# Performance work log

Measured on AMD Instinct MI355X. Metric: run time of the kernel, lower is better.

Reference implementation:

```python
import jax, jax.numpy as jnp
import numpy as np

B, T, A, F_IN = 32, 128, 22, 32
H1, C1 = 4, 128  # heads, gnn_hidden_dim
NEG_SLOPE = 0.2  # GATConv default leaky_relu slope


def setup_inputs() -> dict:
    key = jax.random.key(0)
    ks = jax.random.split(key, 12)
    g = lambda k, shape: jax.random.normal(k, shape, dtype=jnp.float32) * 0.05
    d1 = H1 * C1  # 512, concat output dim of multi-head layers
    return {
        "features": jax.random.normal(ks[0], (B, T, A, F_IN), dtype=jnp.float32),
        "W1": g(ks[1], (F_IN, H1, C1)), "as1": g(ks[2], (H1, C1)), "ad1": g(ks[3], (H1, C1)), "b1": jnp.zeros((d1,), jnp.float32),
        "W2": g(ks[4], (d1, H1, C1)), "as2": g(ks[5], (H1, C1)), "ad2": g(ks[6], (H1, C1)), "b2": jnp.zeros((d1,), jnp.float32),
        "W3": g(ks[7], (d1, 1, C1)), "as3": g(ks[8], (1, C1)), "ad3": g(ks[9], (1, C1)), "b3": jnp.zeros((C1,), jnp.float32),
        "Wc": g(ks[10], (C1, 1)), "bc": jnp.zeros((1,), jnp.float32),
    }


def _gat(x, W, a_src, a_dst, b, concat):
    # x: [G, A, F]; complete graph + self loops == dense attention over all A nodes.
    h = jnp.einsum('gaf,fhc->gahc', x, W)           # [G, A, H, C]
    s = jnp.einsum('gahc,hc->gha', h, a_src)        # att_src . h_j
    d = jnp.einsum('gahc,hc->gha', h, a_dst)        # att_dst . h_i
    logits = d[:, :, :, None] + s[:, :, None, :]    # [G, H, i, j] edge j->i
    logits = jnp.where(logits >= 0, logits, NEG_SLOPE * logits)
    alpha = jax.nn.softmax(logits, axis=-1)         # softmax over source nodes j
    out = jnp.einsum('ghij,gjhc->gihc', alpha, h)   # [G, A, H, C]
    G_, A_, H_, C_ = out.shape
    out = out.reshape(G_, A_, H_ * C_) if concat else out.mean(axis=2)
    return out + b


def reference(features, W1, as1, ad1, b1, W2, as2, ad2, b2, W3, as3, ad3, b3, Wc, bc):
    Bb, Tt, Aa, Ff = features.shape
    x = features.reshape(Bb * Tt, Aa, Ff)           # [G, A, F], G = B*T frame-graphs
    x = jax.nn.relu(_gat(x, W1, as1, ad1, b1, True))
    x = jax.nn.relu(_gat(x, W2, as2, ad2, b2, True))
    x = jax.nn.relu(_gat(x, W3, as3, ad3, b3, False))
    pooled = x.mean(axis=1)                         # global_mean_pool over 22 agents
    return (pooled @ Wc + bc)[:, 0]                 # [G] logits
```

## Files before the change

kernel.cpp:

```cpp
#include <hip/hip_runtime.h>

typedef unsigned short u16;
typedef unsigned int   u32;
typedef unsigned long long u64;
typedef short bf16x8 __attribute__((ext_vector_type(8)));
typedef float f32x4  __attribute__((ext_vector_type(4)));
typedef u32   u32x4  __attribute__((ext_vector_type(4)));

#define NA 22
#define FIN 32
#define XS_STR 520
#define AL_STR 24

#define W1_OFF 0
#define W2_OFF 16384
#define W3_OFF 278528
#define E1_OFF 344064
#define E2_OFF 344576
#define E3_OFF 352768
#define WS_TOTAL 360960

__device__ float b2f(u16 u) {
    return __uint_as_float(((unsigned int)u) << 16);
}

__device__ u16 f2b(float f) {
    unsigned int x = __float_as_uint(f);
    x = (x + 0x7fffu + ((x >> 16) & 1u)) >> 16;
    return (u16)x;
}

__device__ __forceinline__ u32 cvtpk(float lo, float hi) {
    u32 r;
    asm("v_cvt_pk_bf16_f32 %0, %1, %2" : "=v"(r) : "v"(lo), "v"(hi));
    return r;
}

__global__ void swizzle_kernel(const float* W1, const float* W2, const float* W3, u16* ws)
{
    int t = blockIdx.x * 256 + threadIdx.x;
    const float* W; int NT, nshift, base, loc;
    if (t < W2_OFF)      { W = W1; NT = 32; nshift = 9; base = W1_OFF; loc = t; }
    else if (t < W3_OFF) { W = W2; NT = 32; nshift = 9; base = W2_OFF; loc = t - W2_OFF; }
    else if (t < E1_OFF) { W = W3; NT = 8;  nshift = 7; base = W3_OFF; loc = t - W3_OFF; }
    else { return; }
    int k = loc >> nshift;
    int n = loc & ((1 << nshift) - 1);
    u16 v = f2b(W[loc]);
    int kt = k >> 5, quad = (k & 31) >> 3, j = k & 7;
    int nt = n >> 4, lm = n & 15;
    int lane = (quad << 4) | lm;
    ws[base + (((kt * NT + nt) << 9) | (lane << 3) | j)] = v;
}

__global__ void wav_kernel(const float* W1, const float* as1, const float* ad1,
                           const float* W2, const float* as2, const float* ad2,
                           const float* W3, const float* as3, const float* ad3,
                           u16* ws)
{
    int t = blockIdx.x * 256 + threadIdx.x;
    const float* W; const float* asp; const float* adp;
    int H, N, base, loc;
    if (t < 512)        { W = W1; asp = as1; adp = ad1; H = 4; N = 512; base = E1_OFF; loc = t; }
    else if (t < 8704)  { W = W2; asp = as2; adp = ad2; H = 4; N = 512; base = E2_OFF; loc = t - 512; }
    else if (t < 16896) { W = W3; asp = as3; adp = ad3; H = 1; N = 128; base = E3_OFF; loc = t - 8704; }
    else { return; }
    int kt = loc >> 9, r = loc & 511;
    int lane = r >> 3, j = r & 7;
    int quad = lane >> 4, lm = lane & 15;
    u16 outv = 0;
    if (lm < 2 * H) {
        int h = (H == 4) ? (lm & 3) : 0;
        int which = (H == 4) ? (lm >> 2) : lm;
        const float* av = which ? adp : asp;
        int k = kt * 32 + quad * 8 + j;
        float s = 0.f;
        for (int c = 0; c < 128; ++c) { s += W[k * N + h * 128 + c] * av[h * 128 + c]; }
        outv = f2b(s);
    }
    ws[base + (kt << 9) + (lane << 3) + j] = outv;
}


template<int KT, int NT, int NTW, int H>
__device__ __forceinline__ void gat_layer(
    const u16* Wsw, const u16* Wext, const float* bias,
    u16* xs, float* svw, u16* al)
{
    int tid  = threadIdx.x;
    int wave = tid >> 6, lane = tid & 63;
    int quad = lane >> 4, lm = lane & 15;
    int r1 = 16 + lm; if (r1 >= NA) { r1 = lm; }

    f32x4 acc0[NTW], acc1[NTW], accE0, accE1;

    {
        const u16* a0base = xs + lm * XS_STR + quad * 8;
        const u16* a1base = xs + r1 * XS_STR + quad * 8;
        const u16* wbase  = Wsw + ((wave * NTW) << 9) + (lane << 3);
        const u16* ebase  = Wext + (lane << 3);

        f32x4 z4 = {0.f, 0.f, 0.f, 0.f};
        #pragma unroll
        for (int n = 0; n < NTW; ++n) { acc0[n] = z4; acc1[n] = z4; }
        accE0 = z4; accE1 = z4;

        bf16x8 bbuf[2][NTW], ebuf[2], ab0[2], ab1[2];
        #pragma unroll
        for (int n = 0; n < NTW; ++n) { bbuf[0][n] = *(const bf16x8*)(wbase + (n << 9)); }
        ebuf[0] = *(const bf16x8*)(ebase);
        ab0[0] = *(const bf16x8*)(a0base);
        ab1[0] = *(const bf16x8*)(a1base);

        #pragma unroll
        for (int kt = 0; kt < KT; ++kt) {
            const int cur = kt & 1;
            const int nxt = cur ^ 1;
            if (kt + 1 < KT) {
                const u16* wn = wbase + (((kt + 1) * NT) << 9);
                #pragma unroll
                for (int n = 0; n < NTW; ++n) { bbuf[nxt][n] = *(const bf16x8*)(wn + (n << 9)); }
                ebuf[nxt] = *(const bf16x8*)(ebase + ((kt + 1) << 9));
                ab0[nxt] = *(const bf16x8*)(a0base + (kt + 1) * 32);
                ab1[nxt] = *(const bf16x8*)(a1base + (kt + 1) * 32);
            }
            #pragma unroll
            for (int n = 0; n < NTW; ++n) {
                acc0[n] = __builtin_amdgcn_mfma_f32_16x16x32_bf16(ab0[cur], bbuf[cur][n], acc0[n], 0, 0, 0);
                acc1[n] = __builtin_amdgcn_mfma_f32_16x16x32_bf16(ab1[cur], bbuf[cur][n], acc1[n], 0, 0, 0);
            }
            accE0 = __builtin_amdgcn_mfma_f32_16x16x32_bf16(ab0[cur], ebuf[cur], accE0, 0, 0, 0);
            accE1 = __builtin_amdgcn_mfma_f32_16x16x32_bf16(ab1[cur], ebuf[cur], accE1, 0, 0, 0);
        }
    }

    int head = (H == 4) ? (wave >> 1) : 0;
    float* sw = svw + wave * 48;
    if (lm == head) {
        #pragma unroll
        for (int r = 0; r < 4; ++r) {
            sw[quad * 4 + r] = accE0[r];
            int row1 = 16 + quad * 4 + r;
            if (row1 < NA) { sw[row1] = accE1[r]; }
        }
    }
    if (lm == head + H) {
        #pragma unroll
        for (int r = 0; r < 4; ++r) {
            sw[24 + quad * 4 + r] = accE0[r];
            int row1 = 16 + quad * 4 + r;
            if (row1 < NA) { sw[24 + row1] = accE1[r]; }
        }
    }

    bf16x8 bfrag[NTW];
    {
        int s0 = (((quad & 1) << 5) | lm) << 2;
        int s2 = s0 + 64;
        bool hi = (quad >= 2);
        #pragma unroll
        for (int n = 0; n < NTW; ++n) {
            u32 P0a = cvtpk(acc0[n][0], acc0[n][1]);
            u32 P1a = cvtpk(acc0[n][2], acc0[n][3]);
            u32 P0b = cvtpk(acc1[n][0], acc1[n][1]);
            u32 P1b = cvtpk(acc1[n][2], acc1[n][3]);
            u32 w0a = (u32)__builtin_amdgcn_ds_bpermute(s0, (int)P0a);
            u32 w0b = (u32)__builtin_amdgcn_ds_bpermute(s0, (int)P0b);
            u32 w1a = (u32)__builtin_amdgcn_ds_bpermute(s0, (int)P1a);
            u32 w1b = (u32)__builtin_amdgcn_ds_bpermute(s0, (int)P1b);
            u32 w2a = (u32)__builtin_amdgcn_ds_bpermute(s2, (int)P0a);
            u32 w2b = (u32)__builtin_amdgcn_ds_bpermute(s2, (int)P0b);
            u32 w3a = (u32)__builtin_amdgcn_ds_bpermute(s2, (int)P1a);
            union { u32 w[4]; bf16x8 v; } bu;
            bu.w[0] = hi ? w0b : w0a;
            bu.w[1] = hi ? w1b : w1a;
            bu.w[2] = hi ? w2b : w2a;
            bu.w[3] = hi ? 0u  : w3a;
            bfrag[n] = bu.v;
        }
    }

    if (lane < NA) {
        float di = sw[24 + lane];
        float lg[NA];
        float mx = -1.0e30f, ss = 0.0f;
        #pragma unroll
        for (int j = 0; j < NA; ++j) {
            float l = di + sw[j];
            l = fmaxf(l, 0.2f * l);
            lg[j] = l;
            mx = fmaxf(mx, l);
        }
        #pragma unroll
        for (int j = 0; j < NA; ++j) {
            float e = __expf(lg[j] - mx);
            lg[j] = e;
            ss += e;
        }
        float inv = 1.0f / ss;
        u32 pk[12];
        #pragma unroll
        for (int j2 = 0; j2 < 11; ++j2) {
            pk[j2] = cvtpk(lg[2 * j2] * inv, lg[2 * j2 + 1] * inv);
        }
        pk[11] = 0;
        u32* arow = (u32*)(al + (wave * NA + lane) * AL_STR);
        u32x4 q0 = {pk[0], pk[1], pk[2],  pk[3]};
        u32x4 q1 = {pk[4], pk[5], pk[6],  pk[7]};
        u32x4 q2 = {pk[8], pk[9], pk[10], pk[11]};
        *(u32x4*)(arow)     = q0;
        *(u32x4*)(arow + 4) = q1;
        *(u32x4*)(arow + 8) = q2;
    }

    const u16* albase = al + wave * NA * AL_STR;
    bf16x8 zb = {0, 0, 0, 0, 0, 0, 0, 0};
    bf16x8 pa0 = (quad < 3) ? *(const bf16x8*)(albase + lm * AL_STR + quad * 8) : zb;
    bf16x8 pa1 = (quad < 3) ? *(const bf16x8*)(albase + r1 * AL_STR + quad * 8) : zb;

    f32x4 agg0[NTW], agg1[NTW];
    f32x4 z4 = {0.f, 0.f, 0.f, 0.f};
    float bv[NTW];
    #pragma unroll
    for (int n = 0; n < NTW; ++n) {
        int col = (wave * NTW + n) * 16 + lm;
        bv[n] = bias[col];
        agg0[n] = __builtin_amdgcn_mfma_f32_16x16x32_bf16(pa0, bfrag[n], z4, 0, 0, 0);
        agg1[n] = __builtin_amdgcn_mfma_f32_16x16x32_bf16(pa1, bfrag[n], z4, 0, 0, 0);
    }

    __syncthreads();

    #pragma unroll
    for (int n = 0; n < NTW; ++n) {
        int col = (wave * NTW + n) * 16 + lm;
        u16* cbase = xs + col;
        float v0 = fmaxf(agg0[n][0] + bv[n], 0.0f);
        float v1 = fmaxf(agg0[n][1] + bv[n], 0.0f);
        float v2 = fmaxf(agg0[n][2] + bv[n], 0.0f);
        float v3 = fmaxf(agg0[n][3] + bv[n], 0.0f);
        u32 wa0 = cvtpk(v0, v1), wa1 = cvtpk(v2, v3);
        int r0 = quad * 4;
        cbase[(r0 + 0) * XS_STR] = (u16)wa0;
        cbase[(r0 + 1) * XS_STR] = (u16)(wa0 >> 16);
        cbase[(r0 + 2) * XS_STR] = (u16)wa1;
        cbase[(r0 + 3) * XS_STR] = (u16)(wa1 >> 16);
        if (quad < 2) {
            float u0 = fmaxf(agg1[n][0] + bv[n], 0.0f);
            float u1 = fmaxf(agg1[n][1] + bv[n], 0.0f);
            u32 wb0 = cvtpk(u0, u1);
            int r16 = 16 + quad * 4;
            cbase[(r16 + 0) * XS_STR] = (u16)wb0;
            cbase[(r16 + 1) * XS_STR] = (u16)(wb0 >> 16);
            if (quad == 0) {
                float u2 = fmaxf(agg1[n][2] + bv[n], 0.0f);
                float u3 = fmaxf(agg1[n][3] + bv[n], 0.0f);
                u32 wb1 = cvtpk(u2, u3);
                cbase[18 * XS_STR] = (u16)wb1;
                cbase[19 * XS_STR] = (u16)(wb1 >> 16);
            }
        }
    }
    __syncthreads();
}

template<int KT, int NT>
__device__ __forceinline__ void gat_final(
    const u16* Wsw, const u16* Wext, const float* bias,
    const u16* xs, float* svw, u16* al,
    const float* Wc, const float* bc, float* partial, float* out, int g)
{
    int tid  = threadIdx.x;
    int wave = tid >> 6, lane = tid & 63;
    int quad = lane >> 4, lm = lane & 15;
    int r1 = 16 + lm; if (r1 >= NA) { r1 = lm; }

    f32x4 acc0, acc1, accE0, accE1;

    {
        const u16* a0base = xs + lm * XS_STR + quad * 8;
        const u16* a1base = xs + r1 * XS_STR + quad * 8;
        const u16* wbase  = Wsw + (wave << 9) + (lane << 3);
        const u16* ebase  = Wext + (lane << 3);

        f32x4 z4 = {0.f, 0.f, 0.f, 0.f};
        acc0 = z4; acc1 = z4; accE0 = z4; accE1 = z4;

        bf16x8 bbuf[2], ebuf[2], ab0[2], ab1[2];
        bbuf[0] = *(const bf16x8*)(wbase);
        ebuf[0] = *(const bf16x8*)(ebase);
        ab0[0] = *(const bf16x8*)(a0base);
        ab1[0] = *(const bf16x8*)(a1base);

        #pragma unroll
        for (int kt = 0; kt < KT; ++kt) {
            const int cur = kt & 1;
            const int nxt = cur ^ 1;
            if (kt + 1 < KT) {
                bbuf[nxt] = *(const bf16x8*)(wbase + (((kt + 1) * NT) << 9));
                ebuf[nxt] = *(const bf16x8*)(ebase + ((kt + 1) << 9));
                ab0[nxt] = *(const bf16x8*)(a0base + (kt + 1) * 32);
                ab1[nxt] = *(const bf16x8*)(a1base + (kt + 1) * 32);
            }
            acc0  = __builtin_amdgcn_mfma_f32_16x16x32_bf16(ab0[cur], bbuf[cur], acc0, 0, 0, 0);
            acc1  = __builtin_amdgcn_mfma_f32_16x16x32_bf16(ab1[cur], bbuf[cur], acc1, 0, 0, 0);
            accE0 = __builtin_amdgcn_mfma_f32_16x16x32_bf16(ab0[cur], ebuf[cur], accE0, 0, 0, 0);
            accE1 = __builtin_amdgcn_mfma_f32_16x16x32_bf16(ab1[cur], ebuf[cur], accE1, 0, 0, 0);
        }
    }

    float* sw = svw + wave * 48;
    if (lm == 0) {
        #pragma unroll
        for (int r = 0; r < 4; ++r) {
            sw[quad * 4 + r] = accE0[r];
            int row1 = 16 + quad * 4 + r;
            if (row1 < NA) { sw[row1] = accE1[r]; }
        }
    }
    if (lm == 1) {
        #pragma unroll
        for (int r = 0; r < 4; ++r) {
            sw[24 + quad * 4 + r] = accE0[r];
            int row1 = 16 + quad * 4 + r;
            if (row1 < NA) { sw[24 + row1] = accE1[r]; }
        }
    }

    bf16x8 bfrag;
    {
        int s0 = (((quad & 1) << 5) | lm) << 2;
        int s2 = s0 + 64;
        bool hi = (quad >= 2);
        u32 P0a = cvtpk(acc0[0], acc0[1]);
        u32 P1a = cvtpk(acc0[2], acc0[3]);
        u32 P0b = cvtpk(acc1[0], acc1[1]);
        u32 P1b = cvtpk(acc1[2], acc1[3]);
        u32 w0a = (u32)__builtin_amdgcn_ds_bpermute(s0, (int)P0a);
        u32 w0b = (u32)__builtin_amdgcn_ds_bpermute(s0, (int)P0b);
        u32 w1a = (u32)__builtin_amdgcn_ds_bpermute(s0, (int)P1a);
        u32 w1b = (u32)__builtin_amdgcn_ds_bpermute(s0, (int)P1b);
        u32 w2a = (u32)__builtin_amdgcn_ds_bpermute(s2, (int)P0a);
        u32 w2b = (u32)__builtin_amdgcn_ds_bpermute(s2, (int)P0b);
        u32 w3a = (u32)__builtin_amdgcn_ds_bpermute(s2, (int)P1a);
        union { u32 w[4]; bf16x8 v; } bu;
        bu.w[0] = hi ? w0b : w0a;
        bu.w[1] = hi ? w1b : w1a;
        bu.w[2] = hi ? w2b : w2a;
        bu.w[3] = hi ? 0u  : w3a;
        bfrag = bu.v;
    }

    if (lane < NA) {
        float di = sw[24 + lane];
        float lg[NA];
        float mx = -1.0e30f, ss = 0.0f;
        #pragma unroll
        for (int j = 0; j < NA; ++j) {
            float l = di + sw[j];
            l = fmaxf(l, 0.2f * l);
            lg[j] = l;
            mx = fmaxf(mx, l);
        }
        #pragma unroll
        for (int j = 0; j < NA; ++j) {
            float e = __expf(lg[j] - mx);
            lg[j] = e;
            ss += e;
        }
        float inv = 1.0f / ss;
        u32 pk[12];
        #pragma unroll
        for (int j2 = 0; j2 < 11; ++j2) {
            pk[j2] = cvtpk(lg[2 * j2] * inv, lg[2 * j2 + 1] * inv);
        }
        pk[11] = 0;
        u32* arow = (u32*)(al + (wave * NA + lane) * AL_STR);
        u32x4 q0 = {pk[0], pk[1], pk[2],  pk[3]};
        u32x4 q1 = {pk[4], pk[5], pk[6],  pk[7]};
        u32x4 q2 = {pk[8], pk[9], pk[10], pk[11]};
        *(u32x4*)(arow)     = q0;
        *(u32x4*)(arow + 4) = q1;
        *(u32x4*)(arow + 8) = q2;
    }

    const u16* albase = al + wave * NA * AL_STR;
    bf16x8 zb = {0, 0, 0, 0, 0, 0, 0, 0};
    bf16x8 pa0 = (quad < 3) ? *(const bf16x8*)(albase + lm * AL_STR + quad * 8) : zb;
    bf16x8 pa1 = (quad < 3) ? *(const bf16x8*)(albase + r1 * AL_STR + quad * 8) : zb;

    f32x4 z4 = {0.f, 0.f, 0.f, 0.f};
    f32x4 agg0 = __builtin_amdgcn_mfma_f32_16x16x32_bf16(pa0, bfrag, z4, 0, 0, 0);
    f32x4 agg1 = __builtin_amdgcn_mfma_f32_16x16x32_bf16(pa1, bfrag, z4, 0, 0, 0);

    int col = wave * 16 + lm;
    float bvv = bias[col];
    float cs = 0.0f;
    #pragma unroll
    for (int r = 0; r < 4; ++r) { cs += fmaxf(agg0[r] + bvv, 0.0f); }
    #pragma unroll
    for (int r = 0; r < 4; ++r) {
        int row1 = 16 + quad * 4 + r;
        if (row1 < NA) { cs += fmaxf(agg1[r] + bvv, 0.0f); }
    }
    cs += __shfl_xor(cs, 16);
    cs += __shfl_xor(cs, 32);
    float part = (cs / 22.0f) * Wc[col];
    part += __shfl_xor(part, 1);
    part += __shfl_xor(part, 2);
    part += __shfl_xor(part, 4);
    part += __shfl_xor(part, 8);
    if (lane == 0) { partial[wave] = part; }
    __syncthreads();
    if (tid == 0) {
        float t = 0.0f;
        #pragma unroll
        for (int w = 0; w < 8; ++w) { t += partial[w]; }
        out[g] = t + bc[0];
    }
}

__global__ void __launch_bounds__(512, 3)
pressgnn_kernel(const float* feats, const u16* ws,
                const float* b1, const float* b2, const float* b3,
                const float* Wc, const float* bc,
                float* out)
{
    __shared__ __align__(16) u16 xs[NA * XS_STR];
    __shared__ __align__(16) u16 al[8 * NA * AL_STR];
    __shared__ __align__(16) float svw[8 * 48];
    __shared__ float partial[8];

    int g = blockIdx.x;
    int tid = threadIdx.x;

    for (int i = tid; i < NA * FIN; i += 512) {
        int row = i >> 5;
        int col = i & 31;
        xs[row * XS_STR + col] = f2b(feats[g * NA * FIN + i]);
    }
    __syncthreads();

    gat_layer<1,  32, 4, 4>(ws + W1_OFF, ws + E1_OFF, b1, xs, svw, al);
    gat_layer<16, 32, 4, 4>(ws + W2_OFF, ws + E2_OFF, b2, xs, svw, al);
    gat_final<16, 8>(ws + W3_OFF, ws + E3_OFF, b3, xs, svw, al,
                     Wc, bc, partial, out, g);
}

extern "C" void kernel_launch(void* const* d_in, const int* in_sizes, int n_in,
                              void* d_out, int out_size, void* d_ws, size_t ws_size,
                              hipStream_t stream) {
    const float* feats = (const float*)d_in[0];
    const float* W1  = (const float*)d_in[1];
    const float* as1 = (const float*)d_in[2];
    const float* ad1 = (const float*)d_in[3];
    const float* b1  = (const float*)d_in[4];
    const float* W2  = (const float*)d_in[5];
    const float* as2 = (const float*)d_in[6];
    const float* ad2 = (const float*)d_in[7];
    const float* b2  = (const float*)d_in[8];
    const float* W3  = (const float*)d_in[9];
    const float* as3 = (const float*)d_in[10];
    const float* ad3 = (const float*)d_in[11];
    const float* b3  = (const float*)d_in[12];
    const float* Wc  = (const float*)d_in[13];
    const float* bc  = (const float*)d_in[14];
    float* out = (float*)d_out;
    u16* ws = (u16*)d_ws;

    swizzle_kernel<<<dim3(1344), dim3(256), 0, stream>>>(W1, W2, W3, ws);
    wav_kernel<<<dim3(66), dim3(256), 0, stream>>>(W1, as1, ad1, W2, as2, ad2,
                                                   W3, as3, ad3, ws);

    pressgnn_kernel<<<dim3(out_size), dim3(512), 0, stream>>>(
        feats, ws, b1, b2, b3, Wc, bc, out);
}
```

Before: 254.1 us.

## Process two frame-graphs per 1024-thread block to reuse weight fragments

The main kernel now handles two graphs per block with 16 waves. Each weight B-fragment loaded from global memory feeds MFMAs for both graphs, which halves weight traffic per graph. Attention logit MFMAs and softmax run only on lead waves, and the attention matrices are shared across waves through LDS behind an extra barrier. The wav precompute kernel is also rewritten to use wave-parallel dot products with shuffle reductions instead of serial 128-length loops per thread. The cost is a larger block, a bigger LDS footprint and more synchronisation, which may reduce occupancy.

```diff
diff --git a/kernel.cpp b/kernel.cpp
--- a/kernel.cpp
+++ b/kernel.cpp
@@ -10,6 +10,7 @@
 #define NA 22
 #define FIN 32
 #define XS_STR 520
+#define XS_G (NA * XS_STR)
 #define AL_STR 24
 
 #define W1_OFF 0
@@ -19,10 +20,6 @@
 #define E2_OFF 344576
 #define E3_OFF 352768
 #define WS_TOTAL 360960
-
-__device__ float b2f(u16 u) {
-    return __uint_as_float(((unsigned int)u) << 16);
-}
 
 __device__ u16 f2b(float f) {
     unsigned int x = __float_as_uint(f);
@@ -58,32 +55,115 @@
                            const float* W3, const float* as3, const float* ad3,
                            u16* ws)
 {
-    int t = blockIdx.x * 256 + threadIdx.x;
-    const float* W; const float* asp; const float* adp;
-    int H, N, base, loc;
-    if (t < 512)        { W = W1; asp = as1; adp = ad1; H = 4; N = 512; base = E1_OFF; loc = t; }
-    else if (t < 8704)  { W = W2; asp = as2; adp = ad2; H = 4; N = 512; base = E2_OFF; loc = t - 512; }
-    else if (t < 16896) { W = W3; asp = as3; adp = ad3; H = 1; N = 128; base = E3_OFF; loc = t - 8704; }
-    else { return; }
-    int kt = loc >> 9, r = loc & 511;
-    int lane = r >> 3, j = r & 7;
-    int quad = lane >> 4, lm = lane & 15;
-    u16 outv = 0;
-    if (lm < 2 * H) {
-        int h = (H == 4) ? (lm & 3) : 0;
-        int which = (H == 4) ? (lm >> 2) : lm;
-        const float* av = which ? adp : asp;
-        int k = kt * 32 + quad * 8 + j;
-        float s = 0.f;
-        for (int c = 0; c < 128; ++c) { s += W[k * N + h * 128 + c] * av[h * 128 + c]; }
-        outv = f2b(s);
-    }
-    ws[base + (kt << 9) + (lane << 3) + j] = outv;
-}
-
-
-template<int KT, int NT, int NTW, int H>
-__device__ __forceinline__ void gat_layer(
+    int wid = blockIdx.x * 4 + (threadIdx.x >> 6);
+    int lane = threadIdx.x & 63;
+    int grp = lane >> 4, c4 = lane & 15;
+
+    if (wid < 544) {
+        const float* W; const float* asp; const float* adp; int k, base;
+        if (wid < 32) { W = W1; asp = as1; adp = ad1; k = wid;      base = E1_OFF; }
+        else          { W = W2; asp = as2; adp = ad2; k = wid - 32; base = E2_OFF; }
+        int h = grp;
+        const float4* wp = (const float4*)(W + k * 512 + lane * 8);
+        float4 wa = wp[0], wb = wp[1];
+        const float4* sp = (const float4*)(asp + h * 128 + c4 * 8);
+        const float4* dp = (const float4*)(adp + h * 128 + c4 * 8);
+        float4 sa = sp[0], sb = sp[1];
+        float4 da = dp[0], db = dp[1];
+        float ps = wa.x*sa.x + wa.y*sa.y + wa.z*sa.z + wa.w*sa.w
+                 + wb.x*sb.x + wb.y*sb.y + wb.z*sb.z + wb.w*sb.w;
+        float pd = wa.x*da.x + wa.y*da.y + wa.z*da.z + wa.w*da.w
+                 + wb.x*db.x + wb.y*db.y + wb.z*db.z + wb.w*db.w;
+        #pragma unroll
+        for (int off = 1; off <= 8; off <<= 1) {
+            ps += __shfl_xor(ps, off);
+            pd += __shfl_xor(pd, off);
+        }
+        int kt = k >> 5, quad = (k & 31) >> 3, j = k & 7;
+        if (c4 < 4) {
+            int col = c4 * 4 + h;
+            float v = (c4 == 0) ? ps : (c4 == 1) ? pd : 0.0f;
+            ws[base + (kt << 9) + (((quad << 4) | col) << 3) + j] = f2b(v);
+        }
+    } else if (wid < 672) {
+        int k = (wid - 544) * 4 + grp;
+        const float4* wp = (const float4*)(W3 + k * 128 + c4 * 8);
+        float4 wa = wp[0], wb = wp[1];
+        const float4* sp = (const float4*)(as3 + c4 * 8);
+        const float4* dp = (const float4*)(ad3 + c4 * 8);
+        float4 sa = sp[0], sb = sp[1];
+        float4 da = dp[0], db = dp[1];
+        float ps = wa.x*sa.x + wa.y*sa.y + wa.z*sa.z + wa.w*sa.w
+                 + wb.x*sb.x + wb.y*sb.y + wb.z*sb.z + wb.w*sb.w;
+        float pd = wa.x*da.x + wa.y*da.y + wa.z*da.z + wa.w*da.w
+                 + wb.x*db.x + wb.y*db.y + wb.z*db.z + wb.w*db.w;
+        #pragma unroll
+        for (int off = 1; off <= 8; off <<= 1) {
+            ps += __shfl_xor(ps, off);
+            pd += __shfl_xor(pd, off);
+        }
+        int kt = k >> 5, quad = (k & 31) >> 3, j = k & 7;
+        float v = (c4 == 0) ? ps : (c4 == 1) ? pd : 0.0f;
+        ws[E3_OFF + (kt << 9) + (((quad << 4) | c4) << 3) + j] = f2b(v);
+    }
+}
+
+__device__ __forceinline__ bf16x8 xpose(f32x4 a0, f32x4 a1, int s0, int s2, bool hi)
+{
+    u32 P0a = cvtpk(a0[0], a0[1]);
+    u32 P1a = cvtpk(a0[2], a0[3]);
+    u32 P0b = cvtpk(a1[0], a1[1]);
+    u32 P1b = cvtpk(a1[2], a1[3]);
+    u32 w0a = (u32)__builtin_amdgcn_ds_bpermute(s0, (int)P0a);
+    u32 w0b = (u32)__builtin_amdgcn_ds_bpermute(s0, (int)P0b);
+    u32 w1a = (u32)__builtin_amdgcn_ds_bpermute(s0, (int)P1a);
+    u32 w1b = (u32)__builtin_amdgcn_ds_bpermute(s0, (int)P1b);
+    u32 w2a = (u32)__builtin_amdgcn_ds_bpermute(s2, (int)P0a);
+    u32 w2b = (u32)__builtin_amdgcn_ds_bpermute(s2, (int)P0b);
+    u32 w3a = (u32)__builtin_amdgcn_ds_bpermute(s2, (int)P1a);
+    union { u32 w[4]; bf16x8 v; } bu;
+    bu.w[0] = hi ? w0b : w0a;
+    bu.w[1] = hi ? w1b : w1a;
+    bu.w[2] = hi ? w2b : w2a;
+    bu.w[3] = hi ? 0u  : w3a;
+    return bu.v;
+}
+
+__device__ __forceinline__ void softmax_al(const float* sw, u16* al_slot, int lane)
+{
+    if (lane < NA) {
+        float di = sw[24 + lane];
+        float lg[NA];
+        float mx = -1.0e30f, ss = 0.0f;
+        #pragma unroll
+        for (int j = 0; j < NA; ++j) {
+            float l = di + sw[j];
+            l = fmaxf(l, 0.2f * l);
+            lg[j] = l;
+            mx = fmaxf(mx, l);
+        }
+        #pragma unroll
+        for (int j = 0; j < NA; ++j) {
+            float e = __expf(lg[j] - mx);
+            lg[j] = e;
+            ss += e;
+        }
+        float inv = 1.0f / ss;
+        u32 pk[12];
+        #pragma unroll
+        for (int j2 = 0; j2 < 11; ++j2) {
+            pk[j2] = cvtpk(lg[2 * j2] * inv, lg[2 * j2 + 1] * inv);
+        }
+        pk[11] = 0;
+        u32* arow = (u32*)(al_slot + lane * AL_STR);
+        *(u32x4*)(arow)     = (u32x4){pk[0], pk[1], pk[2],  pk[3]};
+        *(u32x4*)(arow + 4) = (u32x4){pk[4], pk[5], pk[6],  pk[7]};
+        *(u32x4*)(arow + 8) = (u32x4){pk[8], pk[9], pk[10], pk[11]};
+    }
+}
+
+template<int KT, int NT>
+__device__ __forceinline__ void gat_layer2(
     const u16* Wsw, const u16* Wext, const float* bias,
     u16* xs, float* svw, u16* al)
 {
@@ -91,26 +171,33 @@
     int wave = tid >> 6, lane = tid & 63;
     int quad = lane >> 4, lm = lane & 15;
     int r1 = 16 + lm; if (r1 >= NA) { r1 = lm; }
-
-    f32x4 acc0[NTW], acc1[NTW], accE0, accE1;
+    bool lead = (wave < 8);
+    int gl = wave & 1, hl = wave >> 1;
+
+    f32x4 acc0[2][2], acc1[2][2], accE0, accE1;
 
     {
-        const u16* a0base = xs + lm * XS_STR + quad * 8;
-        const u16* a1base = xs + r1 * XS_STR + quad * 8;
-        const u16* wbase  = Wsw + ((wave * NTW) << 9) + (lane << 3);
-        const u16* ebase  = Wext + (lane << 3);
+        const u16* a00 = xs + lm * XS_STR + quad * 8;
+        const u16* a10 = xs + r1 * XS_STR + quad * 8;
+        const u16* wbase = Wsw + ((wave * 2) << 9) + (lane << 3);
+        const u16* ebase = Wext + (lane << 3);
 
         f32x4 z4 = {0.f, 0.f, 0.f, 0.f};
         #pragma unroll
-        for (int n = 0; n < NTW; ++n) { acc0[n] = z4; acc1[n] = z4; }
+        for (int g = 0; g < 2; ++g) {
+            acc0[g][0] = z4; acc0[g][1] = z4;
+            acc1[g][0] = z4; acc1[g][1] = z4;
+        }
         accE0 = z4; accE1 = z4;
 
-        bf16x8 bbuf[2][NTW], ebuf[2], ab0[2], ab1[2];
-        #pragma unroll
-        for (int n = 0; n < NTW; ++n) { bbuf[0][n] = *(const bf16x8*)(wbase + (n << 9)); }
-        ebuf[0] = *(const bf16x8*)(ebase);
-        ab0[0] = *(const bf16x8*)(a0base);
-        ab1[0] = *(const bf16x8*)(a1base);
+        bf16x8 bbuf[2][2], ebuf[2], ab0[2][2], ab1[2][2];
+        bbuf[0][0] = *(const bf16x8*)(wbase);
+        bbuf[0][1] = *(const bf16x8*)(wbase + 512);
+        if (lead) { ebuf[0] = *(const bf16x8*)(ebase); }
+        ab0[0][0] = *(const bf16x8*)(a00);
+        ab1[0][0] = *(const bf16x8*)(a10);
+        ab0[0][1] = *(const bf16x8*)(a00 + XS_G);
+        ab1[0][1] = *(const bf16x8*)(a10 + XS_G);
 
         #pragma unroll
         for (int kt = 0; kt < KT; ++kt) {
@@ -118,179 +205,142 @@
             const int nxt = cur ^ 1;
             if (kt + 1 < KT) {
                 const u16* wn = wbase + (((kt + 1) * NT) << 9);
+                bbuf[nxt][0] = *(const bf16x8*)(wn);
+                bbuf[nxt][1] = *(const bf16x8*)(wn + 512);
+                if (lead) { ebuf[nxt] = *(const bf16x8*)(ebase + ((kt + 1) << 9)); }
+                ab0[nxt][0] = *(const bf16x8*)(a00 + (kt + 1) * 32);
+                ab1[nxt][0] = *(const bf16x8*)(a10 + (kt + 1) * 32);
+                ab0[nxt][1] = *(const bf16x8*)(a00 + XS_G + (kt + 1) * 32);
+                ab1[nxt][1] = *(const bf16x8*)(a10 + XS_G + (kt + 1) * 32);
+            }
+            #pragma unroll
+            for (int g = 0; g < 2; ++g) {
                 #pragma unroll
-                for (int n = 0; n < NTW; ++n) { bbuf[nxt][n] = *(const bf16x8*)(wn + (n << 9)); }
-                ebuf[nxt] = *(const bf16x8*)(ebase + ((kt + 1) << 9));
-                ab0[nxt] = *(const bf16x8*)(a0base + (kt + 1) * 32);
-                ab1[nxt] = *(const bf16x8*)(a1base + (kt + 1) * 32);
-            }
+                for (int n = 0; n < 2; ++n) {
+                    acc0[g][n] = __builtin_amdgcn_mfma_f32_16x16x32_bf16(ab0[cur][g], bbuf[cur][n], acc0[g][n], 0, 0, 0);
+                    acc1[g][n] = __builtin_amdgcn_mfma_f32_16x16x32_bf16(ab1[cur][g], bbuf[cur][n], acc1[g][n], 0, 0, 0);
+                }
+            }
+            if (lead) {
+                bf16x8 ea0 = gl ? ab0[cur][1] : ab0[cur][0];
+                bf16x8 ea1 = gl ? ab1[cur][1] : ab1[cur][0];
+                accE0 = __builtin_amdgcn_mfma_f32_16x16x32_bf16(ea0, ebuf[cur], accE0, 0, 0, 0);
+                accE1 = __builtin_amdgcn_mfma_f32_16x16x32_bf16(ea1, ebuf[cur], accE1, 0, 0, 0);
+            }
+        }
+    }
+
+    if (lead) {
+        float* sw = svw + wave * 48;
+        if (lm == hl) {
             #pragma unroll
-            for (int n = 0; n < NTW; ++n) {
-                acc0[n] = __builtin_amdgcn_mfma_f32_16x16x32_bf16(ab0[cur], bbuf[cur][n], acc0[n], 0, 0, 0);
-                acc1[n] = __builtin_amdgcn_mfma_f32_16x16x32_bf16(ab1[cur], bbuf[cur][n], acc1[n], 0, 0, 0);
-            }
-            accE0 = __builtin_amdgcn_mfma_f32_16x16x32_bf16(ab0[cur], ebuf[cur], accE0, 0, 0, 0);
-            accE1 = __builtin_amdgcn_mfma_f32_16x16x32_bf16(ab1[cur], ebuf[cur], accE1, 0, 0, 0);
-        }
-    }
-
-    int head = (H == 4) ? (wave >> 1) : 0;
-    float* sw = svw + wave * 48;
-    if (lm == head) {
-        #pragma unroll
-        for (int r = 0; r < 4; ++r) {
-            sw[quad * 4 + r] = accE0[r];
-            int row1 = 16 + quad * 4 + r;
-            if (row1 < NA) { sw[row1] = accE1[r]; }
-        }
-    }
-    if (lm == head + H) {
-        #pragma unroll
-        for (int r = 0; r < 4; ++r) {
-            sw[24 + quad * 4 + r] = accE0[r];
-            int row1 = 16 + quad * 4 + r;
-            if (row1 < NA) { sw[24 + row1] = accE1[r]; }
-        }
-    }
-
-    bf16x8 bfrag[NTW];
+            for (int r = 0; r < 4; ++r) {
+                sw[quad * 4 + r] = accE0[r];
+                int row1 = 16 + quad * 4 + r;
+                if (row1 < NA) { sw[row1] = accE1[r]; }
+            }
+        }
+        if (lm == hl + 4) {
+            #pragma unroll
+            for (int r = 0; r < 4; ++r) {
+                sw[24 + quad * 4 + r] = accE0[r];
+                int row1 = 16 + quad * 4 + r;
+                if (row1 < NA) { sw[24 + row1] = accE1[r]; }
+            }
+        }
+        softmax_al(sw, al + (gl * 4 + hl) * NA * AL_STR, lane);
+    }
+
+    bf16x8 bfrag[2][2];
     {
         int s0 = (((quad & 1) << 5) | lm) << 2;
         int s2 = s0 + 64;
         bool hi = (quad >= 2);
         #pragma unroll
-        for (int n = 0; n < NTW; ++n) {
-            u32 P0a = cvtpk(acc0[n][0], acc0[n][1]);
-            u32 P1a = cvtpk(acc0[n][2], acc0[n][3]);
-            u32 P0b = cvtpk(acc1[n][0], acc1[n][1]);
-            u32 P1b = cvtpk(acc1[n][2], acc1[n][3]);
-            u32 w0a = (u32)__builtin_amdgcn_ds_bpermute(s0, (int)P0a);
-            u32 w0b = (u32)__builtin_amdgcn_ds_bpermute(s0, (int)P0b);
-            u32 w1a = (u32)__builtin_amdgcn_ds_bpermute(s0, (int)P1a);
-            u32 w1b = (u32)__builtin_amdgcn_ds_bpermute(s0, (int)P1b);
-            u32 w2a = (u32)__builtin_amdgcn_ds_bpermute(s2, (int)P0a);
-            u32 w2b = (u32)__builtin_amdgcn_ds_bpermute(s2, (int)P0b);
-            u32 w3a = (u32)__builtin_amdgcn_ds_bpermute(s2, (int)P1a);
-            union { u32 w[4]; bf16x8 v; } bu;
-            bu.w[0] = hi ? w0b : w0a;
-            bu.w[1] = hi ? w1b : w1a;
-            bu.w[2] = hi ? w2b : w2a;
-            bu.w[3] = hi ? 0u  : w3a;
-            bfrag[n] = bu.v;
-        }
-    }
-
-    if (lane < NA) {
-        float di = sw[24 + lane];
-        float lg[NA];
-        float mx = -1.0e30f, ss = 0.0f;
-        #pragma unroll
-        for (int j = 0; j < NA; ++j) {
-            float l = di + sw[j];
-            l = fmaxf(l, 0.2f * l);
-            lg[j] = l;
-            mx = fmaxf(mx, l);
-        }
-        #pragma unroll
-        for (int j = 0; j < NA; ++j) {
-            float e = __expf(lg[j] - mx);
-            lg[j] = e;
-            ss += e;
-        }
-        float inv = 1.0f / ss;
-        u32 pk[12];
-        #pragma unroll
-        for (int j2 = 0; j2 < 11; ++j2) {
-            pk[j2] = cvtpk(lg[2 * j2] * inv, lg[2 * j2 + 1] * inv);
-        }
-        pk[11] = 0;
-        u32* arow = (u32*)(al + (wave * NA + lane) * AL_STR);
-        u32x4 q0 = {pk[0], pk[1], pk[2],  pk[3]};
-        u32x4 q1 = {pk[4], pk[5], pk[6],  pk[7]};
-        u32x4 q2 = {pk[8], pk[9], pk[10], pk[11]};
-        *(u32x4*)(arow)     = q0;
-        *(u32x4*)(arow + 4) = q1;
-        *(u32x4*)(arow + 8) = q2;
-    }
-
-    const u16* albase = al + wave * NA * AL_STR;
-    bf16x8 zb = {0, 0, 0, 0, 0, 0, 0, 0};
-    bf16x8 pa0 = (quad < 3) ? *(const bf16x8*)(albase + lm * AL_STR + quad * 8) : zb;
-    bf16x8 pa1 = (quad < 3) ? *(const bf16x8*)(albase + r1 * AL_STR + quad * 8) : zb;
-
-    f32x4 agg0[NTW], agg1[NTW];
-    f32x4 z4 = {0.f, 0.f, 0.f, 0.f};
-    float bv[NTW];
+        for (int g = 0; g < 2; ++g) {
+            bfrag[g][0] = xpose(acc0[g][0], acc1[g][0], s0, s2, hi);
+            bfrag[g][1] = xpose(acc0[g][1], acc1[g][1], s0, s2, hi);
+        }
+    }
+
+    __syncthreads();
+
+    int head = wave >> 2;
     #pragma unroll
-    for (int n = 0; n < NTW; ++n) {
-        int col = (wave * NTW + n) * 16 + lm;
-        bv[n] = bias[col];
-        agg0[n] = __builtin_amdgcn_mfma_f32_16x16x32_bf16(pa0, bfrag[n], z4, 0, 0, 0);
-        agg1[n] = __builtin_amdgcn_mfma_f32_16x16x32_bf16(pa1, bfrag[n], z4, 0, 0, 0);
-    }
-
+    for (int g = 0; g < 2; ++g) {
+        const u16* alb = al + (g * 4 + head) * NA * AL_STR;
+        bf16x8 zb = {0, 0, 0, 0, 0, 0, 0, 0};
+        bf16x8 pa0 = (quad < 3) ? *(const bf16x8*)(alb + lm * AL_STR + quad * 8) : zb;
+        bf16x8 pa1 = (quad < 3) ? *(const bf16x8*)(alb + r1 * AL_STR + quad * 8) : zb;
+        u16* xg = xs + g * XS_G;
+        #pragma unroll
+        for (int n = 0; n < 2; ++n) {
+            int col = (wave * 2 + n) * 16 + lm;
+            float bv = bias[col];
+            f32x4 z4 = {0.f, 0.f, 0.f, 0.f};
+            f32x4 agg0 = __builtin_amdgcn_mfma_f32_16x16x32_bf16(pa0, bfrag[g][n], z4, 0, 0, 0);
+            f32x4 agg1 = __builtin_amdgcn_mfma_f32_16x16x32_bf16(pa1, bfrag[g][n], z4, 0, 0, 0);
+            u16* cbase = xg + col;
+            float v0 = fmaxf(agg0[0] + bv, 0.0f);
+            float v1 = fmaxf(agg0[1] + bv, 0.0f);
+            float v2 = fmaxf(agg0[2] + bv, 0.0f);
+            float v3 = fmaxf(agg0[3] + bv, 0.0f);
+            u32 wa0 = cvtpk(v0, v1), wa1 = cvtpk(v2, v3);
+            int r0 = quad * 4;
+            cbase[(r0 + 0) * XS_STR] = (u16)wa0;
+            cbase[(r0 + 1) * XS_STR] = (u16)(wa0 >> 16);
+            cbase[(r0 + 2) * XS_STR] = (u16)wa1;
+            cbase[(r0 + 3) * XS_STR] = (u16)(wa1 >> 16);
+            if (quad < 2) {
+                float u0 = fmaxf(agg1[0] + bv, 0.0f);
+                float u1 = fmaxf(agg1[1] + bv, 0.0f);
+                u32 wb0 = cvtpk(u0, u1);
+                int r16 = 16 + quad * 4;
+                cbase[(r16 + 0) * XS_STR] = (u16)wb0;
+                cbase[(r16 + 1) * XS_STR] = (u16)(wb0 >> 16);
+                if (quad == 0) {
+                    float u2 = fmaxf(agg1[2] + bv, 0.0f);
+                    float u3 = fmaxf(agg1[3] + bv, 0.0f);
+                    u32 wb1 = cvtpk(u2, u3);
+                    cbase[18 * XS_STR] = (u16)wb1;
+                    cbase[19 * XS_STR] = (u16)(wb1 >> 16);
+                }
+            }
+        }
+    }
     __syncthreads();
-
-    #pragma unroll
-    for (int n = 0; n < NTW; ++n) {
-        int col = (wave * NTW + n) * 16 + lm;
-        u16* cbase = xs + col;
-        float v0 = fmaxf(agg0[n][0] + bv[n], 0.0f);
-        float v1 = fmaxf(agg0[n][1] + bv[n], 0.0f);
-        float v2 = fmaxf(agg0[n][2] + bv[n], 0.0f);
-        float v3 = fmaxf(agg0[n][3] + bv[n], 0.0f);
-        u32 wa0 = cvtpk(v0, v1), wa1 = cvtpk(v2, v3);
-        int r0 = quad * 4;
-        cbase[(r0 + 0) * XS_STR] = (u16)wa0;
-        cbase[(r0 + 1) * XS_STR] = (u16)(wa0 >> 16);
-        cbase[(r0 + 2) * XS_STR] = (u16)wa1;
-        cbase[(r0 + 3) * XS_STR] = (u16)(wa1 >> 16);
-        if (quad < 2) {
-            float u0 = fmaxf(agg1[n][0] + bv[n], 0.0f);
-            float u1 = fmaxf(agg1[n][1] + bv[n], 0.0f);
-            u32 wb0 = cvtpk(u0, u1);
-            int r16 = 16 + quad * 4;
-            cbase[(r16 + 0) * XS_STR] = (u16)wb0;
-            cbase[(r16 + 1) * XS_STR] = (u16)(wb0 >> 16);
-            if (quad == 0) {
-                float u2 = fmaxf(agg1[n][2] + bv[n], 0.0f);
-                float u3 = fmaxf(agg1[n][3] + bv[n], 0.0f);
-                u32 wb1 = cvtpk(u2, u3);
-                cbase[18 * XS_STR] = (u16)wb1;
-                cbase[19 * XS_STR] = (u16)(wb1 >> 16);
-            }
-        }
-    }
-    __syncthreads();
 }
 
 template<int KT, int NT>
-__device__ __forceinline__ void gat_final(
+__device__ __forceinline__ void gat_final2(
     const u16* Wsw, const u16* Wext, const float* bias,
     const u16* xs, float* svw, u16* al,
-    const float* Wc, const float* bc, float* partial, float* out, int g)
+    const float* Wc, const float* bc, float* partial, float* out,
+    int g0, int ng)
 {
     int tid  = threadIdx.x;
     int wave = tid >> 6, lane = tid & 63;
     int quad = lane >> 4, lm = lane & 15;
     int r1 = 16 + lm; if (r1 >= NA) { r1 = lm; }
+    int gsel = wave >> 3, nt = wave & 7;
+    bool lead = (nt == 0);
+    const u16* xg = xs + gsel * XS_G;
 
     f32x4 acc0, acc1, accE0, accE1;
-
     {
-        const u16* a0base = xs + lm * XS_STR + quad * 8;
-        const u16* a1base = xs + r1 * XS_STR + quad * 8;
-        const u16* wbase  = Wsw + (wave << 9) + (lane << 3);
-        const u16* ebase  = Wext + (lane << 3);
+        const u16* a00 = xg + lm * XS_STR + quad * 8;
+        const u16* a10 = xg + r1 * XS_STR + quad * 8;
+        const u16* wbase = Wsw + (nt << 9) + (lane << 3);
+        const u16* ebase = Wext + (lane << 3);
 
         f32x4 z4 = {0.f, 0.f, 0.f, 0.f};
         acc0 = z4; acc1 = z4; accE0 = z4; accE1 = z4;
 
         bf16x8 bbuf[2], ebuf[2], ab0[2], ab1[2];
         bbuf[0] = *(const bf16x8*)(wbase);
-        ebuf[0] = *(const bf16x8*)(ebase);
-        ab0[0] = *(const bf16x8*)(a0base);
-        ab1[0] = *(const bf16x8*)(a1base);
+        if (lead) { ebuf[0] = *(const bf16x8*)(ebase); }
+        ab0[0] = *(const bf16x8*)(a00);
+        ab1[0] = *(const bf16x8*)(a10);
 
         #pragma unroll
         for (int kt = 0; kt < KT; ++kt) {
@@ -298,33 +348,38 @@
             const int nxt = cur ^ 1;
             if (kt + 1 < KT) {
                 bbuf[nxt] = *(const bf16x8*)(wbase + (((kt + 1) * NT) << 9));
-                ebuf[nxt] = *(const bf16x8*)(ebase + ((kt + 1) << 9));
-                ab0[nxt] = *(const bf16x8*)(a0base + (kt + 1) * 32);
-                ab1[nxt] = *(const bf16x8*)(a1base + (kt + 1) * 32);
-            }
-            acc0  = __builtin_amdgcn_mfma_f32_16x16x32_bf16(ab0[cur], bbuf[cur], acc0, 0, 0, 0);
-            acc1  = __builtin_amdgcn_mfma_f32_16x16x32_bf16(ab1[cur], bbuf[cur], acc1, 0, 0, 0);
-            accE0 = __builtin_amdgcn_mfma_f32_16x16x32_bf16(ab0[cur], ebuf[cur], accE0, 0, 0, 0);
-            accE1 = __builtin_amdgcn_mfma_f32_16x16x32_bf16(ab1[cur], ebuf[cur], accE1, 0, 0, 0);
-        }
-    }
-
-    float* sw = svw + wave * 48;
-    if (lm == 0) {
-        #pragma unroll
-        for (int r = 0; r < 4; ++r) {
-            sw[quad * 4 + r] = accE0[r];
-            int row1 = 16 + quad * 4 + r;
-            if (row1 < NA) { sw[row1] = accE1[r]; }
-        }
-    }
-    if (lm == 1) {
-        #pragma unroll
-        for (int r = 0; r < 4; ++r) {
-            sw[24 + quad * 4 + r] = accE0[r];
-            int row1 = 16 + quad * 4 + r;
-            if (row1 < NA) { sw[24 + row1] = accE1[r]; }
-        }
+                if (lead) { ebuf[nxt] = *(const bf16x8*)(ebase + ((kt + 1) << 9)); }
+                ab0[nxt] = *(const bf16x8*)(a00 + (kt + 1) * 32);
+                ab1[nxt] = *(const bf16x8*)(a10 + (kt + 1) * 32);
+            }
+            acc0 = __builtin_amdgcn_mfma_f32_16x16x32_bf16(ab0[cur], bbuf[cur], acc0, 0, 0, 0);
+            acc1 = __builtin_amdgcn_mfma_f32_16x16x32_bf16(ab1[cur], bbuf[cur], acc1, 0, 0, 0);
+            if (lead) {
+                accE0 = __builtin_amdgcn_mfma_f32_16x16x32_bf16(ab0[cur], ebuf[cur], accE0, 0, 0, 0);
+                accE1 = __builtin_amdgcn_mfma_f32_16x16x32_bf16(ab1[cur], ebuf[cur], accE1, 0, 0, 0);
+            }
+        }
+    }
+
+    if (lead) {
+        float* sw = svw + wave * 48;
+        if (lm == 0) {
+            #pragma unroll
+            for (int r = 0; r < 4; ++r) {
+                sw[quad * 4 + r] = accE0[r];
+                int row1 = 16 + quad * 4 + r;
+                if (row1 < NA) { sw[row1] = accE1[r]; }
+            }
+        }
+        if (lm == 1) {
+            #pragma unroll
+            for (int r = 0; r < 4; ++r) {
+                sw[24 + quad * 4 + r] = accE0[r];
+                int row1 = 16 + quad * 4 + r;
+                if (row1 < NA) { sw[24 + row1] = accE1[r]; }
+            }
+        }
+        softmax_al(sw, al + (gsel * 4) * NA * AL_STR, lane);
     }
 
     bf16x8 bfrag;
@@ -332,68 +387,21 @@
         int s0 = (((quad & 1) << 5) | lm) << 2;
         int s2 = s0 + 64;
         bool hi = (quad >= 2);
-        u32 P0a = cvtpk(acc0[0], acc0[1]);
-        u32 P1a = cvtpk(acc0[2], acc0[3]);
-        u32 P0b = cvtpk(acc1[0], acc1[1]);
-        u32 P1b = cvtpk(acc1[2], acc1[3]);
-        u32 w0a = (u32)__builtin_amdgcn_ds_bpermute(s0, (int)P0a);
-        u32 w0b = (u32)__builtin_amdgcn_ds_bpermute(s0, (int)P0b);
-        u32 w1a = (u32)__builtin_amdgcn_ds_bpermute(s0, (int)P1a);
-        u32 w1b = (u32)__builtin_amdgcn_ds_bpermute(s0, (int)P1b);
-        u32 w2a = (u32)__builtin_amdgcn_ds_bpermute(s2, (int)P0a);
-        u32 w2b = (u32)__builtin_amdgcn_ds_bpermute(s2, (int)P0b);
-        u32 w3a = (u32)__builtin_amdgcn_ds_bpermute(s2, (int)P1a);
-        union { u32 w[4]; bf16x8 v; } bu;
-        bu.w[0] = hi ? w0b : w0a;
-        bu.w[1] = hi ? w1b : w1a;
-        bu.w[2] = hi ? w2b : w2a;
-        bu.w[3] = hi ? 0u  : w3a;
-        bfrag = bu.v;
-    }
-
-    if (lane < NA) {
-        float di = sw[24 + lane];
-        float lg[NA];
-        float mx = -1.0e30f, ss = 0.0f;
-        #pragma unroll
-        for (int j = 0; j < NA; ++j) {
-            float l = di + sw[j];
-            l = fmaxf(l, 0.2f * l);
-            lg[j] = l;
-            mx = fmaxf(mx, l);
-        }
-        #pragma unroll
-        for (int j = 0; j < NA; ++j) {
-            float e = __expf(lg[j] - mx);
-            lg[j] = e;
-            ss += e;
-        }
-        float inv = 1.0f / ss;
-        u32 pk[12];
-        #pragma unroll
-        for (int j2 = 0; j2 < 11; ++j2) {
-            pk[j2] = cvtpk(lg[2 * j2] * inv, lg[2 * j2 + 1] * inv);
-        }
-        pk[11] = 0;
-        u32* arow = (u32*)(al + (wave * NA + lane) * AL_STR);
-        u32x4 q0 = {pk[0], pk[1], pk[2],  pk[3]};
-        u32x4 q1 = {pk[4], pk[5], pk[6],  pk[7]};
-        u32x4 q2 = {pk[8], pk[9], pk[10], pk[11]};
-        *(u32x4*)(arow)     = q0;
-        *(u32x4*)(arow + 4) = q1;
-        *(u32x4*)(arow + 8) = q2;
-    }
-
-    const u16* albase = al + wave * NA * AL_STR;
+        bfrag = xpose(acc0, acc1, s0, s2, hi);
+    }
+
+    __syncthreads();
+
+    const u16* alb = al + (gsel * 4) * NA * AL_STR;
     bf16x8 zb = {0, 0, 0, 0, 0, 0, 0, 0};
-    bf16x8 pa0 = (quad < 3) ? *(const bf16x8*)(albase + lm * AL_STR + quad * 8) : zb;
-    bf16x8 pa1 = (quad < 3) ? *(const bf16x8*)(albase + r1 * AL_STR + quad * 8) : zb;
+    bf16x8 pa0 = (quad < 3) ? *(const bf16x8*)(alb + lm * AL_STR + quad * 8) : zb;
+    bf16x8 pa1 = (quad < 3) ? *(const bf16x8*)(alb + r1 * AL_STR + quad * 8) : zb;
 
     f32x4 z4 = {0.f, 0.f, 0.f, 0.f};
     f32x4 agg0 = __builtin_amdgcn_mfma_f32_16x16x32_bf16(pa0, bfrag, z4, 0, 0, 0);
     f32x4 agg1 = __builtin_amdgcn_mfma_f32_16x16x32_bf16(pa1, bfrag, z4, 0, 0, 0);
 
-    int col = wave * 16 + lm;
+    int col = nt * 16 + lm;
     float bvv = bias[col];
     float cs = 0.0f;
     #pragma unroll
@@ -412,39 +420,42 @@
     part += __shfl_xor(part, 8);
     if (lane == 0) { partial[wave] = part; }
     __syncthreads();
-    if (tid == 0) {
+    if (tid < 2 && g0 + tid < ng) {
         float t = 0.0f;
         #pragma unroll
-        for (int w = 0; w < 8; ++w) { t += partial[w]; }
-        out[g] = t + bc[0];
-    }
-}
-
-__global__ void __launch_bounds__(512, 3)
+        for (int w = 0; w < 8; ++w) { t += partial[tid * 8 + w]; }
+        out[g0 + tid] = t + bc[0];
+    }
+}
+
+__global__ void __launch_bounds__(1024, 4)
 pressgnn_kernel(const float* feats, const u16* ws,
                 const float* b1, const float* b2, const float* b3,
                 const float* Wc, const float* bc,
-                float* out)
-{
-    __shared__ __align__(16) u16 xs[NA * XS_STR];
+                float* out, int ng)
+{
+    __shared__ __align__(16) u16 xs[2 * XS_G];
     __shared__ __align__(16) u16 al[8 * NA * AL_STR];
-    __shared__ __align__(16) float svw[8 * 48];
-    __shared__ float partial[8];
-
-    int g = blockIdx.x;
+    __shared__ __align__(16) float svw[16 * 48];
+    __shared__ float partial[16];
+
+    int g0 = blockIdx.x * 2;
     int tid = threadIdx.x;
-
-    for (int i = tid; i < NA * FIN; i += 512) {
-        int row = i >> 5;
-        int col = i & 31;
-        xs[row * XS_STR + col] = f2b(feats[g * NA * FIN + i]);
+    int ng2 = ng - g0; if (ng2 > 2) ng2 = 2;
+
+    for (int i = tid; i < 2 * NA * FIN; i += 1024) {
+        int g = (i >= NA * FIN) ? 1 : 0;
+        int loc = i - g * NA * FIN;
+        int row = loc >> 5, c = loc & 31;
+        float v = (g < ng2) ? feats[(g0 + g) * (NA * FIN) + loc] : 0.0f;
+        xs[g * XS_G + row * XS_STR + c] = f2b(v);
     }
     __syncthreads();
 
-    gat_layer<1,  32, 4, 4>(ws + W1_OFF, ws + E1_OFF, b1, xs, svw, al);
-    gat_layer<16, 32, 4, 4>(ws + W2_OFF, ws + E2_OFF, b2, xs, svw, al);
-    gat_final<16, 8>(ws + W3_OFF, ws + E3_OFF, b3, xs, svw, al,
-                     Wc, bc, partial, out, g);
+    gat_layer2<1,  32>(ws + W1_OFF, ws + E1_OFF, b1, xs, svw, al);
+    gat_layer2<16, 32>(ws + W2_OFF, ws + E2_OFF, b2, xs, svw, al);
+    gat_final2<16, 8>(ws + W3_OFF, ws + E3_OFF, b3, xs, svw, al,
+                      Wc, bc, partial, out, g0, ng);
 }
 
 extern "C" void kernel_launch(void* const* d_in, const int* in_sizes, int n_in,
@@ -469,9 +480,10 @@
     u16* ws = (u16*)d_ws;
 
     swizzle_kernel<<<dim3(1344), dim3(256), 0, stream>>>(W1, W2, W3, ws);
-    wav_kernel<<<dim3(66), dim3(256), 0, stream>>>(W1, as1, ad1, W2, as2, ad2,
-                                                   W3, as3, ad3, ws);
-
-    pressgnn_kernel<<<dim3(out_size), dim3(512), 0, stream>>>(
-        feats, ws, b1, b2, b3, Wc, bc, out);
-}
+    wav_kernel<<<dim3(168), dim3(256), 0, stream>>>(W1, as1, ad1, W2, as2, ad2,
+                                                    W3, as3, ad3, ws);
+
+    int nblk = (out_size + 1) / 2;
+    pressgnn_kernel<<<dim3(nblk), dim3(1024), 0, stream>>>(
+        feats, ws, b1, b2, b3, Wc, bc, out, out_size);
+}
```

New measurement: 520.2 us. 105% more time.
